# Kernel optimization log

Measured on AMD Instinct MI355X. Metric: run time of the kernel, lower is better.

Reference implementation:

```python
import jax, jax.numpy as jnp
import numpy as np

N_NODES = 100000
N_EDGES = 3200000
IN_DIM = 256
OUT_DIM = 64


def setup_inputs() -> dict:
    key = jax.random.key(0)
    k1, k2, k3 = jax.random.split(key, 3)
    h = jax.random.normal(k1, (N_NODES, IN_DIM), dtype=jnp.float32)
    W = jax.random.normal(k2, (IN_DIM, OUT_DIM), dtype=jnp.float32) * (IN_DIM ** -0.5)
    b = jnp.zeros((OUT_DIM,), dtype=jnp.float32)
    edges = jax.random.randint(k3, (2, N_EDGES), 0, N_NODES, dtype=jnp.int64)
    return {"h": h, "W": W, "b": b, "edges": edges}


def reference(h, W, b, edges):
    # DGL GraphConv, norm='both':
    #   out = D_dst^{-1/2} * A * (D_src^{-1/2} * (h @ W)) + b
    # degrees clamped to min 1; then log_softmax over classes.
    N = h.shape[0]
    src, dst = edges[0], edges[1]
    ones = jnp.ones(src.shape, dtype=h.dtype)
    out_deg = jax.ops.segment_sum(ones, src, num_segments=N)
    in_deg = jax.ops.segment_sum(ones, dst, num_segments=N)
    norm_src = jnp.maximum(out_deg, 1.0) ** -0.5  # [N]
    norm_dst = jnp.maximum(in_deg, 1.0) ** -0.5   # [N]
    # in_dim > out_dim: project first (matches DGL's mult-first optimization)
    m = (h @ W) * norm_src[:, None]               # [N, out_dim]
    agg = jax.ops.segment_sum(m[src], dst, num_segments=N)  # SpMM
    out = agg * norm_dst[:, None] + b
    return jax.nn.log_softmax(out, axis=1)
```

## Files before the change

kernel.cpp:

```cpp
#include <hip/hip_runtime.h>
#include <hip/hip_fp16.h>
#include <math.h>

#define IN_DIM 256
#define OUT_DIM 64
#define BROWS 256
#define GROWS 128
#define SC_THREADS 512
#define SC_EPB 16
#define SC_EDGES (SC_THREADS * SC_EPB)
#define BM 128
#define KC 32
#define HS_LD 33
#define CSR_CAP 5120

__global__ void __launch_bounds__(SC_THREADS) scatter_pairs_kernel(
        const int* __restrict__ src, const int* __restrict__ dst,
        int* __restrict__ dcursor, int* __restrict__ scursor,
        unsigned* __restrict__ pairs, unsigned char* __restrict__ sbytes,
        int n_edges, int nb, int cap) {
    __shared__ int lhd[512];
    __shared__ int lbd[512];
    __shared__ int lod[512];
    __shared__ int lhs[512];
    __shared__ int lbs[512];
    __shared__ int los[512];
    __shared__ unsigned stp[SC_EDGES];
    __shared__ unsigned char stb[SC_EDGES];

    const int t = threadIdx.x;
    const int wave = t >> 6;
    const int lane = t & 63;

    lhd[t] = 0; lhs[t] = 0;
    __syncthreads();

    const int base = blockIdx.x * SC_EDGES;
    int s[SC_EPB], d[SC_EPB];
    if (base + SC_EDGES <= n_edges) {
        const int4* s4 = (const int4*)(src + base);
        const int4* d4 = (const int4*)(dst + base);
        #pragma unroll
        for (int j = 0; j < SC_EPB / 4; ++j) {
            int4 a = s4[j * SC_THREADS + t];
            int4 c = d4[j * SC_THREADS + t];
            s[4*j+0] = a.x; s[4*j+1] = a.y; s[4*j+2] = a.z; s[4*j+3] = a.w;
            d[4*j+0] = c.x; d[4*j+1] = c.y; d[4*j+2] = c.z; d[4*j+3] = c.w;
        }
        #pragma unroll
        for (int i = 0; i < SC_EPB; ++i) {
            atomicAdd(&lhd[d[i] >> 8], 1);
            atomicAdd(&lhs[s[i] >> 8], 1);
        }
    } else {
        #pragma unroll
        for (int i = 0; i < SC_EPB; ++i) {
            int e = base + i * SC_THREADS + t;
            if (e < n_edges) {
                s[i] = src[e];
                d[i] = dst[e];
                atomicAdd(&lhd[d[i] >> 8], 1);
                atomicAdd(&lhs[s[i] >> 8], 1);
            } else {
                s[i] = -1; d[i] = 0;
            }
        }
    }
    __syncthreads();

    for (int i = t; i < nb; i += SC_THREADS) {
        int c = lhd[i];
        lbd[i] = c ? atomicAdd(&dcursor[i], c) : 0;
        c = lhs[i];
        lbs[i] = c ? atomicAdd(&scursor[i], c) : 0;
    }

    {
        int vd = (t < nb) ? lhd[t] : 0;
        int vs = (t < nb) ? lhs[t] : 0;
        lod[t] = vd; los[t] = vs;
        __syncthreads();
        #pragma unroll
        for (int dd = 1; dd < 512; dd <<= 1) {
            int td = (t >= dd) ? lod[t - dd] : 0;
            int ts = (t >= dd) ? los[t - dd] : 0;
            __syncthreads();
            lod[t] += td; los[t] += ts;
            __syncthreads();
        }
        lod[t] -= vd; los[t] -= vs;
    }
    __syncthreads();

    #pragma unroll
    for (int i = 0; i < SC_EPB; ++i) {
        if (s[i] >= 0) {
            int bkt = d[i] >> 8;
            int pos = atomicAdd(&lod[bkt], 1);
            stp[pos] = ((unsigned)s[i] << 8) | (unsigned)(d[i] & 255);
            int sb = s[i] >> 8;
            int spos = atomicAdd(&los[sb], 1);
            stb[spos] = (unsigned char)(s[i] & 255);
        }
    }
    __syncthreads();

    for (int b2 = wave; b2 < nb; b2 += SC_THREADS / 64) {
        int cnt = lhd[b2];
        if (cnt) {
            int st = lod[b2] - cnt;
            int gb = lbd[b2];
            unsigned* gp = pairs + (size_t)b2 * cap;
            for (int j = lane; j < cnt; j += 64)
                if (gb + j < cap) gp[gb + j] = stp[st + j];
        }
        cnt = lhs[b2];
        if (cnt) {
            int st = los[b2] - cnt;
            int gb = lbs[b2];
            unsigned char* gp = sbytes + (size_t)b2 * cap;
            for (int j = lane; j < cnt; j += 64)
                if (gb + j < cap) gp[gb + j] = stb[st + j];
        }
    }
}

__global__ void __launch_bounds__(256) count_src_kernel(
        const unsigned char* __restrict__ sbytes, const int* __restrict__ scursor,
        int* __restrict__ out_deg, int n_nodes, int cap) {
    __shared__ int cnt[BROWS];
    cnt[threadIdx.x] = 0;
    __syncthreads();
    const int beg = blockIdx.x * cap;
    int len = scursor[blockIdx.x];
    if (len > cap) len = cap;
    const int end = beg + len;
    for (int i = beg + threadIdx.x; i < end; i += 256)
        atomicAdd(&cnt[sbytes[i]], 1);
    __syncthreads();
    const int row = blockIdx.x * BROWS + threadIdx.x;
    if (row < n_nodes) out_deg[row] = cnt[threadIdx.x];
}

__global__ void __launch_bounds__(256) gemm_kernel(
        const float* __restrict__ h, const float* __restrict__ W,
        const int* __restrict__ out_deg, __half* __restrict__ m, int n_nodes) {
    __shared__ float hs[BM * HS_LD];
    __shared__ float Ws[KC * OUT_DIM];

    const int t = threadIdx.x;
    const int c = t & 15;
    const int g = t >> 4;
    const int rowBase = blockIdx.x * BM;

    float acc[8][4];
    #pragma unroll
    for (int i = 0; i < 8; ++i)
        #pragma unroll
        for (int j = 0; j < 4; ++j) acc[i][j] = 0.f;

    for (int kc = 0; kc < IN_DIM / KC; ++kc) {
        __syncthreads();
        #pragma unroll
        for (int i = 0; i < 4; ++i) {
            int idx = t + 256 * i;
            int row = idx >> 3;
            int seg = idx & 7;
            int grow = rowBase + row;
            float4 v = make_float4(0.f, 0.f, 0.f, 0.f);
            if (grow < n_nodes)
                v = *(const float4*)(h + (size_t)grow * IN_DIM + kc * KC + seg * 4);
            float* dp = &hs[row * HS_LD + seg * 4];
            dp[0] = v.x; dp[1] = v.y; dp[2] = v.z; dp[3] = v.w;
        }
        {
            const float4* Wg = (const float4*)(W + kc * KC * OUT_DIM);
            float4* Wl = (float4*)Ws;
            Wl[t] = Wg[t];
            Wl[t + 256] = Wg[t + 256];
        }
        __syncthreads();

        #pragma unroll 4
        for (int kk = 0; kk < KC; ++kk) {
            float4 bv = *(const float4*)&Ws[kk * OUT_DIM + c * 4];
            #pragma unroll
            for (int i = 0; i < 8; ++i) {
                float a = hs[(g * 8 + i) * HS_LD + kk];
                acc[i][0] += a * bv.x;
                acc[i][1] += a * bv.y;
                acc[i][2] += a * bv.z;
                acc[i][3] += a * bv.w;
            }
        }
    }

    #pragma unroll
    for (int i = 0; i < 8; ++i) {
        int row = rowBase + g * 8 + i;
        if (row < n_nodes) {
            float nr = rsqrtf(fmaxf((float)out_deg[row], 1.0f));
            union { __half2 h2[2]; uint2 u; } pk;
            pk.h2[0] = __floats2half2_rn(acc[i][0] * nr, acc[i][1] * nr);
            pk.h2[1] = __floats2half2_rn(acc[i][2] * nr, acc[i][3] * nr);
            *(uint2*)(m + (size_t)row * OUT_DIM + c * 4) = pk.u;
        }
    }
}

__global__ void __launch_bounds__(512) bucket_gather_kernel(
        const unsigned* __restrict__ pairs, const int* __restrict__ dcursor,
        const __half* __restrict__ m, const float* __restrict__ b,
        float* __restrict__ out, int n_nodes, int cap) {
    __shared__ int cnt[GROWS];
    __shared__ int rofs[GROWS];
    __shared__ int cur[GROWS];
    __shared__ int csr[CSR_CAP];

    const int t = threadIdx.x;
    const int bkt = blockIdx.x >> 1;
    const int hsel = blockIdx.x & 1;
    const unsigned hbit = (unsigned)hsel << 7;
    const int beg = bkt * cap;
    int len = dcursor[bkt];
    if (len > cap) len = cap;
    const int end = beg + len;
    const int rowBase = bkt * BROWS + hsel * GROWS;

    const int wave = t >> 6;
    const int lane = t & 63;
    const int half = lane >> 5;
    const int c    = lane & 31;
    const __half2* __restrict__ m2 = (const __half2*)m;
    const float2 bb = *(const float2*)(b + 2 * c);

    if (t < GROWS) cnt[t] = 0;
    __syncthreads();

    for (int i = beg + t; i < end; i += 512) {
        unsigned p = pairs[i];
        if ((p & 128u) == hbit) atomicAdd(&cnt[p & 127u], 1);
    }
    __syncthreads();
    if (t < GROWS) rofs[t] = cnt[t];
    __syncthreads();
    #pragma unroll
    for (int d = 1; d < GROWS; d <<= 1) {
        int tv = (t < GROWS && t >= d) ? rofs[t - d] : 0;
        __syncthreads();
        if (t < GROWS) rofs[t] += tv;
        __syncthreads();
    }
    if (t < GROWS) cur[t] = rofs[t] - cnt[t];
    __syncthreads();
    const int tot = rofs[GROWS - 1];

    if (tot <= CSR_CAP) {
        for (int i = beg + t; i < end; i += 512) {
            unsigned p = pairs[i];
            if ((p & 128u) == hbit) {
                int pos = atomicAdd(&cur[p & 127u], 1);
                csr[pos] = (int)(p >> 8);
            }
        }
        __syncthreads();
        for (int r = wave; r < GROWS; r += 8) {
            const int row = rowBase + r;
            if (row >= n_nodes) continue;
            const int cend = rofs[r];
            const int cbeg = cend - cnt[r];
            float ax = 0.f, ay = 0.f;
            int i = cbeg;
            for (; i + 16 <= cend; i += 16) {
                int s[8];
                #pragma unroll
                for (int k = 0; k < 8; ++k) s[k] = csr[i + 2 * k + half];
                #pragma unroll
                for (int k = 0; k < 8; ++k) {
                    float2 f = __half22float2(m2[(unsigned)(s[k] * (OUT_DIM / 2) + c)]);
                    ax += f.x; ay += f.y;
                }
            }
            for (int e = i + half; e < cend; e += 2) {
                float2 f = __half22float2(m2[(unsigned)(csr[e] * (OUT_DIM / 2) + c)]);
                ax += f.x; ay += f.y;
            }
            ax += __shfl_xor(ax, 32, 64);
            ay += __shfl_xor(ay, 32, 64);

            float nd = rsqrtf(fmaxf((float)cnt[r], 1.0f));
            float x0 = ax * nd + bb.x;
            float x1 = ay * nd + bb.y;
            float mx = fmaxf(x0, x1);
            #pragma unroll
            for (int o = 16; o > 0; o >>= 1) mx = fmaxf(mx, __shfl_xor(mx, o, 64));
            float ex0 = expf(x0 - mx), ex1 = expf(x1 - mx);
            float sm = ex0 + ex1;
            #pragma unroll
            for (int o = 16; o > 0; o >>= 1) sm += __shfl_xor(sm, o, 64);
            float ls = logf(sm);
            if (half == 0)
                *(float2*)(out + (size_t)row * OUT_DIM + 2 * c) =
                    make_float2(x0 - mx - ls, x1 - mx - ls);
        }
    } else {
        for (int r = wave; r < GROWS; r += 8) {
            const int row = rowBase + r;
            if (row >= n_nodes) continue;
            const unsigned match = (unsigned)(hsel * GROWS + r);
            float ax = 0.f, ay = 0.f;
            for (int e = beg; e < end; ++e) {
                unsigned p = pairs[e];
                if ((p & 255u) == match) {
                    float2 f = __half22float2(m2[(unsigned)((p >> 8) * (OUT_DIM / 2) + c)]);
                    ax += f.x; ay += f.y;
                }
            }
            float nd = rsqrtf(fmaxf((float)cnt[r], 1.0f));
            float x0 = ax * nd + bb.x;
            float x1 = ay * nd + bb.y;
            float mx = fmaxf(x0, x1);
            #pragma unroll
            for (int o = 16; o > 0; o >>= 1) mx = fmaxf(mx, __shfl_xor(mx, o, 64));
            float ex0 = expf(x0 - mx), ex1 = expf(x1 - mx);
            float sm = ex0 + ex1;
            #pragma unroll
            for (int o = 16; o > 0; o >>= 1) sm += __shfl_xor(sm, o, 64);
            float ls = logf(sm);
            if (half == 0)
                *(float2*)(out + (size_t)row * OUT_DIM + 2 * c) =
                    make_float2(x0 - mx - ls, x1 - mx - ls);
        }
    }
}

static inline size_t align16(size_t x) { return (x + 15) & ~(size_t)15; }

extern "C" void kernel_launch(void* const* d_in, const int* in_sizes, int n_in,
                              void* d_out, int out_size, void* d_ws, size_t ws_size,
                              hipStream_t stream) {
    const float* h = (const float*)d_in[0];
    const float* W = (const float*)d_in[1];
    const float* b = (const float*)d_in[2];
    const int* edges = (const int*)d_in[3];

    const int out_dim = in_sizes[2];
    const int in_dim  = in_sizes[1] / out_dim;
    const int n_nodes = in_sizes[0] / in_dim;
    const int n_edges = in_sizes[3] / 2;

    const int* src = edges;
    const int* dst = edges + n_edges;

    float* out = (float*)d_out;

    const int nb = (n_nodes + BROWS - 1) / BROWS;

    const int epb = (n_edges + nb - 1) / nb;
    const int cap = (epb + (epb >> 2) + 1023 + 1023) & ~1023;

    char* ws = (char*)d_ws;
    size_t off = 0;
    int* out_deg     = (int*)(ws + off); off = align16(off + (size_t)n_nodes * 4);
    int* dcursor     = (int*)(ws + off); off = align16(off + (size_t)nb * 4);
    int* scursor     = (int*)(ws + off); off = align16(off + (size_t)nb * 4);
    __half* m        = (__half*)(ws + off); off = align16(off + (size_t)n_nodes * OUT_DIM * 2);
    unsigned* pairs  = (unsigned*)(ws + off); off = align16(off + (size_t)nb * cap * 4);
    unsigned char* sbytes = (unsigned char*)m;

    (void)hipMemsetAsync(dcursor, 0,
                         (size_t)((char*)(scursor + nb) - (char*)dcursor), stream);

    const int sc_blocks = (n_edges + SC_EDGES - 1) / SC_EDGES;

    scatter_pairs_kernel<<<sc_blocks, SC_THREADS, 0, stream>>>(
        src, dst, dcursor, scursor, pairs, sbytes, n_edges, nb, cap);
    count_src_kernel<<<nb, 256, 0, stream>>>(sbytes, scursor, out_deg, n_nodes, cap);

    gemm_kernel<<<(n_nodes + BM - 1) / BM, 256, 0, stream>>>(h, W, out_deg, m, n_nodes);

    bucket_gather_kernel<<<2 * nb, 512, 0, stream>>>(pairs, dcursor, m, b, out,
                                                     n_nodes, cap);
}
```

Measured before the change: 358.9 us.

## Use fp16 MFMA for the node projection GEMM

Rewrites the h@W projection kernel to convert h and W tiles to fp16 in shared memory and compute with 16x16x16 MFMA instructions instead of fp32 scalar FMAs. The k-chunk grows to 64, and W is stored transposed in LDS. The aim is to cut the compute cost of the GEMM, which may then be bound by streaming h from memory. The trade-off is lower input precision (fp16 operands with fp32 accumulation) and a strided scalar transpose load of W.

Result: no change. 358.8 us (-0.0%).

```diff
diff --git a/kernel.cpp b/kernel.cpp
--- a/kernel.cpp
+++ b/kernel.cpp
@@ -10,9 +10,12 @@
 #define SC_EPB 16
 #define SC_EDGES (SC_THREADS * SC_EPB)
 #define BM 128
-#define KC 32
-#define HS_LD 33
+#define KC2 64
+#define LDH 68
 #define CSR_CAP 5120
+
+typedef _Float16 f16x4 __attribute__((ext_vector_type(4)));
+typedef float f32x4 __attribute__((ext_vector_type(4)));
 
 __global__ void __launch_bounds__(SC_THREADS) scatter_pairs_kernel(
         const int* __restrict__ src, const int* __restrict__ dst,
@@ -145,65 +148,80 @@
 __global__ void __launch_bounds__(256) gemm_kernel(
         const float* __restrict__ h, const float* __restrict__ W,
         const int* __restrict__ out_deg, __half* __restrict__ m, int n_nodes) {
-    __shared__ float hs[BM * HS_LD];
-    __shared__ float Ws[KC * OUT_DIM];
+    __shared__ _Float16 hs[BM * LDH];
+    __shared__ _Float16 Wt[OUT_DIM * LDH];
 
     const int t = threadIdx.x;
-    const int c = t & 15;
-    const int g = t >> 4;
+    const int wave = t >> 6;
+    const int lane = t & 63;
+    const int lg = lane >> 4;
+    const int li = lane & 15;
     const int rowBase = blockIdx.x * BM;
 
-    float acc[8][4];
+    f32x4 acc[2][4];
     #pragma unroll
-    for (int i = 0; i < 8; ++i)
-        #pragma unroll
-        for (int j = 0; j < 4; ++j) acc[i][j] = 0.f;
-
-    for (int kc = 0; kc < IN_DIM / KC; ++kc) {
-        __syncthreads();
-        #pragma unroll
-        for (int i = 0; i < 4; ++i) {
+    for (int rt = 0; rt < 2; ++rt)
+        #pragma unroll
+        for (int ct = 0; ct < 4; ++ct)
+            acc[rt][ct] = (f32x4){0.f, 0.f, 0.f, 0.f};
+
+    for (int kc = 0; kc < IN_DIM / KC2; ++kc) {
+        __syncthreads();
+        #pragma unroll
+        for (int i = 0; i < 8; ++i) {
             int idx = t + 256 * i;
-            int row = idx >> 3;
-            int seg = idx & 7;
-            int grow = rowBase + row;
+            int row = idx >> 4;
+            int s4 = idx & 15;
             float4 v = make_float4(0.f, 0.f, 0.f, 0.f);
-            if (grow < n_nodes)
-                v = *(const float4*)(h + (size_t)grow * IN_DIM + kc * KC + seg * 4);
-            float* dp = &hs[row * HS_LD + seg * 4];
-            dp[0] = v.x; dp[1] = v.y; dp[2] = v.z; dp[3] = v.w;
-        }
-        {
-            const float4* Wg = (const float4*)(W + kc * KC * OUT_DIM);
-            float4* Wl = (float4*)Ws;
-            Wl[t] = Wg[t];
-            Wl[t + 256] = Wg[t + 256];
-        }
-        __syncthreads();
-
-        #pragma unroll 4
-        for (int kk = 0; kk < KC; ++kk) {
-            float4 bv = *(const float4*)&Ws[kk * OUT_DIM + c * 4];
-            #pragma unroll
-            for (int i = 0; i < 8; ++i) {
-                float a = hs[(g * 8 + i) * HS_LD + kk];
-                acc[i][0] += a * bv.x;
-                acc[i][1] += a * bv.y;
-                acc[i][2] += a * bv.z;
-                acc[i][3] += a * bv.w;
-            }
+            if (rowBase + row < n_nodes)
+                v = *(const float4*)(h + (size_t)(rowBase + row) * IN_DIM
+                                     + kc * KC2 + s4 * 4);
+            _Float16* dp = &hs[row * LDH + s4 * 4];
+            dp[0] = (_Float16)v.x; dp[1] = (_Float16)v.y;
+            dp[2] = (_Float16)v.z; dp[3] = (_Float16)v.w;
+        }
+        #pragma unroll
+        for (int i = 0; i < 16; ++i) {
+            int idx = t + 256 * i;
+            int k = idx >> 6;
+            int n = idx & 63;
+            Wt[n * LDH + k] = (_Float16)W[(size_t)(kc * KC2 + k) * OUT_DIM + n];
+        }
+        __syncthreads();
+
+        #pragma unroll
+        for (int ks = 0; ks < KC2 / 16; ++ks) {
+            const int k0 = ks * 16 + lg * 4;
+            f16x4 b0 = *(const f16x4*)&hs[((wave * 2 + 0) * 16 + li) * LDH + k0];
+            f16x4 b1 = *(const f16x4*)&hs[((wave * 2 + 1) * 16 + li) * LDH + k0];
+            f16x4 a0 = *(const f16x4*)&Wt[(0 * 16 + li) * LDH + k0];
+            f16x4 a1 = *(const f16x4*)&Wt[(1 * 16 + li) * LDH + k0];
+            f16x4 a2 = *(const f16x4*)&Wt[(2 * 16 + li) * LDH + k0];
+            f16x4 a3 = *(const f16x4*)&Wt[(3 * 16 + li) * LDH + k0];
+            acc[0][0] = __builtin_amdgcn_mfma_f32_16x16x16f16(a0, b0, acc[0][0], 0, 0, 0);
+            acc[0][1] = __builtin_amdgcn_mfma_f32_16x16x16f16(a1, b0, acc[0][1], 0, 0, 0);
+            acc[0][2] = __builtin_amdgcn_mfma_f32_16x16x16f16(a2, b0, acc[0][2], 0, 0, 0);
+            acc[0][3] = __builtin_amdgcn_mfma_f32_16x16x16f16(a3, b0, acc[0][3], 0, 0, 0);
+            acc[1][0] = __builtin_amdgcn_mfma_f32_16x16x16f16(a0, b1, acc[1][0], 0, 0, 0);
+            acc[1][1] = __builtin_amdgcn_mfma_f32_16x16x16f16(a1, b1, acc[1][1], 0, 0, 0);
+            acc[1][2] = __builtin_amdgcn_mfma_f32_16x16x16f16(a2, b1, acc[1][2], 0, 0, 0);
+            acc[1][3] = __builtin_amdgcn_mfma_f32_16x16x16f16(a3, b1, acc[1][3], 0, 0, 0);
         }
     }
 
     #pragma unroll
-    for (int i = 0; i < 8; ++i) {
-        int row = rowBase + g * 8 + i;
+    for (int rt = 0; rt < 2; ++rt) {
+        int row = rowBase + (wave * 2 + rt) * 16 + li;
         if (row < n_nodes) {
             float nr = rsqrtf(fmaxf((float)out_deg[row], 1.0f));
-            union { __half2 h2[2]; uint2 u; } pk;
-            pk.h2[0] = __floats2half2_rn(acc[i][0] * nr, acc[i][1] * nr);
-            pk.h2[1] = __floats2half2_rn(acc[i][2] * nr, acc[i][3] * nr);
-            *(uint2*)(m + (size_t)row * OUT_DIM + c * 4) = pk.u;
+            #pragma unroll
+            for (int ct = 0; ct < 4; ++ct) {
+                f32x4 dv = acc[rt][ct];
+                union { __half2 h2[2]; uint2 u; } pk;
+                pk.h2[0] = __floats2half2_rn(dv[0] * nr, dv[1] * nr);
+                pk.h2[1] = __floats2half2_rn(dv[2] * nr, dv[3] * nr);
+                *(uint2*)(m + (size_t)row * OUT_DIM + ct * 16 + lg * 4) = pk.u;
+            }
         }
     }
 }
```
